# Kernel tuning notes

Hardware: AMD Instinct MI355X
Metric: run time of the kernel (lower is better)

## Reference

```python
import jax, jax.numpy as jnp
import numpy as np

GROUPS = 16
EPS = 1e-5


def _dcn_v2(x, offset, mask, weight):
    """Modulated deformable 3x3 conv, stride=1, pad=1, no bias.
    x: [B,C,H,W], offset: [B,18,H,W] (dy,dx interleaved per kernel point),
    mask: [B,9,H,W] (modulation scalars), weight: [O,C,3,3]."""
    B, C, H, W = x.shape
    O = weight.shape[0]
    K = 9
    # kernel-point displacements, row-major (kh, kw): k = kh*3 + kw
    ky = jnp.repeat(jnp.arange(3) - 1, 3).astype(x.dtype)   # [9]
    kx = jnp.tile(jnp.arange(3) - 1, 3).astype(x.dtype)      # [9]
    dy = offset[:, 0::2]  # [B,9,H,W]
    dx = offset[:, 1::2]  # [B,9,H,W]
    hh = jnp.arange(H, dtype=x.dtype)
    ww = jnp.arange(W, dtype=x.dtype)
    # sampling coordinates (stride=1, pad=1)
    ys = hh[None, None, :, None] + ky[None, :, None, None] + dy  # [B,9,H,W]
    xs = ww[None, None, None, :] + kx[None, :, None, None] + dx  # [B,9,H,W]

    y0 = jnp.floor(ys)
    x0 = jnp.floor(xs)
    wy1 = ys - y0
    wx1 = xs - x0
    y0i = y0.astype(jnp.int32)
    x0i = x0.astype(jnp.int32)

    flat = x.reshape(B, C, H * W)

    def gather(yi, xi, w):
        # yi, xi, w: [B,9,H,W]; zero-padding outside the image
        valid = (yi >= 0) & (yi < H) & (xi >= 0) & (xi < W)
        idx = jnp.clip(yi, 0, H - 1) * W + jnp.clip(xi, 0, W - 1)  # [B,9,H,W]
        g = jnp.take_along_axis(flat, idx.reshape(B, 1, K * H * W), axis=2)
        g = g.reshape(B, C, K, H, W)
        return g * (w * valid.astype(x.dtype))[:, None]  # [B,C,9,H,W]

    val = (gather(y0i,     x0i,     (1 - wy1) * (1 - wx1))
         + gather(y0i,     x0i + 1, (1 - wy1) * wx1)
         + gather(y0i + 1, x0i,     wy1 * (1 - wx1))
         + gather(y0i + 1, x0i + 1, wy1 * wx1))
    val = val * mask[:, None]  # modulation
    # implicit GEMM: [B,C,9,H,W] x [O,C,9] -> [B,O,H,W]
    return jnp.einsum('bckhw,ock->bohw', val, weight.reshape(O, C, K))


def _group_norm(x, gamma, beta):
    B, C, H, W = x.shape
    xg = x.reshape(B, GROUPS, C // GROUPS, H, W)
    mu = xg.mean(axis=(2, 3, 4), keepdims=True)
    var = xg.var(axis=(2, 3, 4), keepdims=True)
    xn = ((xg - mu) * jax.lax.rsqrt(var + EPS)).reshape(B, C, H, W)
    return xn * gamma[None, :, None, None] + beta[None, :, None, None]


def setup_inputs() -> dict:
    key = jax.random.key(0)
    k1, k2, k3, k4 = jax.random.split(key, 4)
    B, C, O, H, W = 8, 256, 256, 64, 64
    x = jax.random.normal(k1, (B, C, H, W), dtype=jnp.float32)
    offset = jax.random.normal(k2, (B, 18, H, W), dtype=jnp.float32)
    mask = jax.random.uniform(k3, (B, 9, H, W), dtype=jnp.float32)
    weight = jax.random.normal(k4, (O, C, 3, 3), dtype=jnp.float32) * (1.0 / np.sqrt(C * 9))
    gamma = jnp.ones((O,), dtype=jnp.float32)
    beta = jnp.zeros((O,), dtype=jnp.float32)
    return {"x": x, "offset": offset, "mask": mask, "weight": weight,
            "gamma": gamma, "beta": beta}


def reference(x, offset, mask, weight, gamma, beta):
    out = _dcn_v2(x, offset, mask, weight)
    return _group_norm(out, gamma, beta)
```

## Files before the change

kernel.cpp:

```cpp
#include <hip/hip_runtime.h>
#include <stdint.h>


#define B_ 8
#define C_ 256
#define O_ 256
#define H_ 64
#define W_ 64
#define HW_ 4096
#define KTOT 2304
#define GROUPS_ 16
#define EPS_ 1e-5f
#define NSTEP 36
#define VROW 72

typedef float  f32x4  __attribute__((ext_vector_type(4)));
typedef short  short8 __attribute__((ext_vector_type(8)));
typedef unsigned int   u32;
typedef unsigned short u16;

#define XT_BYTES (B_*HW_*C_*2)
#define WIMG_OFF  XT_BYTES
#define WIMG_BYTES (72*16*64*16)
#define STATS_OFF (WIMG_OFF + WIMG_BYTES)

__device__ __forceinline__ u32 bf16r(float f) {
    u32 u = __float_as_uint(f);
    return (u + 0x7fffu + ((u >> 16) & 1u)) >> 16;
}
__device__ __forceinline__ u32 pack_bf16x2(float lo, float hi) {
    return bf16r(lo) | (bf16r(hi) << 16);
}
__device__ __forceinline__ float bflo(u32 u) { return __uint_as_float(u << 16); }
__device__ __forceinline__ float bfhi(u32 u) { return __uint_as_float(u & 0xffff0000u); }

__global__ void k_prep(const float* __restrict__ x, u16* __restrict__ xt,
                       const float* __restrict__ w, u16* __restrict__ wimg) {
    __shared__ float tile[32][33];
    const int bid = blockIdx.x;
    const int tid = threadIdx.x;
    if (bid < 8192) {
        const int pt = bid & 127, ct = (bid >> 7) & 7, b = bid >> 10;
        const int tx = tid & 31, ty = tid >> 5;
        const int p = pt * 32 + tx;
#pragma unroll
        for (int i = 0; i < 4; ++i) {
            int c = ct * 32 + ty + i * 8;
            tile[ty + i * 8][tx] = x[(((size_t)b * C_ + c) << 12) + p];
        }
        __syncthreads();
        const int cp = tx & 15;
        const int ps = ty + (tx >> 4) * 8;
#pragma unroll
        for (int i = 0; i < 2; ++i) {
            const int pl = ps + i * 16;
            u32 v = pack_bf16x2(tile[2 * cp][pl], tile[2 * cp + 1][pl]);
            *(u32*)&xt[((((size_t)b << 12) + pt * 32 + pl) << 8) + ct * 32 + 2 * cp] = v;
        }
    } else {
        const int sub = bid - 8192;
        const int k  = sub >> 3;
        const int c0 = (sub & 7) * 32;
#pragma unroll
        for (int i = 0; i < 4; ++i) {
            const int item = tid + i * 256;
            const int lane = item & 63;
            const int frag = item >> 6;
            const int col = lane & 15, quad = lane >> 4;
            const int n = frag * 16 + col;
            const float* src = w + (size_t)n * KTOT + (size_t)(c0 + quad * 8) * 9 + k;
            u32 o[4];
#pragma unroll
            for (int j = 0; j < 4; ++j)
                o[j] = pack_bf16x2(src[(size_t)(2 * j) * 9], src[(size_t)(2 * j + 1) * 9]);
            *(uint4*)&wimg[((size_t)sub * 1024 + item) * 8] = *(uint4*)o;
        }
    }
}

__device__ __forceinline__ void issue_gather(const u16* __restrict__ xtb,
                                             const float* __restrict__ mwp,
                                             const int* __restrict__ mip,
                                             int c0, int gpos, int oct,
                                             uint4 g[8], f32x4& mw) {
    mw = *(const f32x4*)&mwp[gpos * 4];
    const int4 ix = *(const int4*)&mip[gpos * 4];
    const u16* cb = xtb + c0 + oct * 16;
    const u16* p0 = cb + ((size_t)ix.x << 8);
    const u16* p1 = cb + ((size_t)ix.y << 8);
    const u16* p2 = cb + ((size_t)ix.z << 8);
    const u16* p3 = cb + ((size_t)ix.w << 8);
    g[0] = *(const uint4*)p0; g[1] = *(const uint4*)(p0 + 8);
    g[2] = *(const uint4*)p1; g[3] = *(const uint4*)(p1 + 8);
    g[4] = *(const uint4*)p2; g[5] = *(const uint4*)(p2 + 8);
    g[6] = *(const uint4*)p3; g[7] = *(const uint4*)(p3 + 8);
}

__device__ __forceinline__ void interp_store(const uint4 g[8], f32x4 mw, u16* dst) {
    float s[16];
#pragma unroll
    for (int i = 0; i < 16; ++i) s[i] = 0.f;
    const float ww[4] = {mw.x, mw.y, mw.z, mw.w};
#pragma unroll
    for (int cr = 0; cr < 4; ++cr) {
        const float wg = ww[cr];
        const uint4 a = g[2 * cr], bq = g[2 * cr + 1];
        s[0] += wg * bflo(a.x);  s[1] += wg * bfhi(a.x);
        s[2] += wg * bflo(a.y);  s[3] += wg * bfhi(a.y);
        s[4] += wg * bflo(a.z);  s[5] += wg * bfhi(a.z);
        s[6] += wg * bflo(a.w);  s[7] += wg * bfhi(a.w);
        s[8]  += wg * bflo(bq.x); s[9]  += wg * bfhi(bq.x);
        s[10] += wg * bflo(bq.y); s[11] += wg * bfhi(bq.y);
        s[12] += wg * bflo(bq.z); s[13] += wg * bfhi(bq.z);
        s[14] += wg * bflo(bq.w); s[15] += wg * bfhi(bq.w);
    }
    uint4 pk0, pk1;
    pk0.x = pack_bf16x2(s[0], s[1]);   pk0.y = pack_bf16x2(s[2], s[3]);
    pk0.z = pack_bf16x2(s[4], s[5]);   pk0.w = pack_bf16x2(s[6], s[7]);
    pk1.x = pack_bf16x2(s[8], s[9]);   pk1.y = pack_bf16x2(s[10], s[11]);
    pk1.z = pack_bf16x2(s[12], s[13]); pk1.w = pack_bf16x2(s[14], s[15]);
    *(uint4*)dst = pk0;
    *(uint4*)(dst + 8) = pk1;
}

__device__ __forceinline__ void load_wfrags(const u16* __restrict__ wimg, int sub0,
                                            int wid, int lane, short8 bfp[8]) {
#pragma unroll
    for (int kc = 0; kc < 2; ++kc)
#pragma unroll
        for (int ni = 0; ni < 4; ++ni)
            bfp[kc * 4 + ni] = *(const short8*)
                &wimg[(((size_t)(sub0 + kc) * 16 + wid * 4 + ni) * 64 + lane) * 8];
}

__launch_bounds__(256, 2)
__global__ void k_dcn(const u16* __restrict__ xt, const u16* __restrict__ wimg,
                      const float* __restrict__ offp, const float* __restrict__ mskp,
                      float* __restrict__ out, float* __restrict__ stats) {
    __shared__ __align__(16) float meta_w[9 * 64 * 4];
    __shared__ __align__(16) int   meta_i[9 * 64 * 4];
    __shared__ __align__(16) u16   lds_v[2][64 * VROW];

    const int tid = threadIdx.x;
    const int gid = blockIdx.x;
    const int b   = gid & 7;
    const int m0  = (gid >> 3) * 64;
    const int lane = tid & 63, wid = tid >> 6;
    const int col = lane & 15, quad = lane >> 4;
    const int gpos = tid >> 2, oct = tid & 3;

    const u16* xtb = xt + ((size_t)b << 20);

    for (int it = tid; it < 576; it += 256) {
        const int pos = it & 63, k = it >> 6;
        const int pg = m0 + pos;
        const int hh = pg >> 6, wwi = pg & 63;
        const float dy = offp[((size_t)(b * 18 + 2 * k) << 12) + pg];
        const float dx = offp[((size_t)(b * 18 + 2 * k + 1) << 12) + pg];
        const float mv = mskp[((size_t)(b * 9 + k) << 12) + pg];
        const float ys = (float)(hh + (k / 3) - 1) + dy;
        const float xs = (float)(wwi + (k % 3) - 1) + dx;
        const float y0f = floorf(ys), x0f = floorf(xs);
        const int y0 = (int)y0f, x0 = (int)x0f;
        const float wy1 = ys - y0f, wx1 = xs - x0f;
        const float wy0 = 1.f - wy1, wx0 = 1.f - wx1;
        const int y1 = y0 + 1, x1 = x0 + 1;
        const float vy0 = (y0 >= 0 && y0 < H_) ? 1.f : 0.f;
        const float vy1 = (y1 >= 0 && y1 < H_) ? 1.f : 0.f;
        const float vx0 = (x0 >= 0 && x0 < W_) ? 1.f : 0.f;
        const float vx1 = (x1 >= 0 && x1 < W_) ? 1.f : 0.f;
        const int y0c = min(max(y0, 0), H_ - 1), y1c = min(max(y1, 0), H_ - 1);
        const int x0c = min(max(x0, 0), W_ - 1), x1c = min(max(x1, 0), W_ - 1);
        meta_w[it * 4 + 0] = mv * wy0 * wx0 * vy0 * vx0;
        meta_w[it * 4 + 1] = mv * wy0 * wx1 * vy0 * vx1;
        meta_w[it * 4 + 2] = mv * wy1 * wx0 * vy1 * vx0;
        meta_w[it * 4 + 3] = mv * wy1 * wx1 * vy1 * vx1;
        meta_i[it * 4 + 0] = y0c * W_ + x0c;
        meta_i[it * 4 + 1] = y0c * W_ + x1c;
        meta_i[it * 4 + 2] = y1c * W_ + x0c;
        meta_i[it * 4 + 3] = y1c * W_ + x1c;
    }
    __syncthreads();

    uint4 g[8]; f32x4 mw; short8 bfp[8];
    issue_gather(xtb, &meta_w[0], &meta_i[0], 0, gpos, oct, g, mw);
    load_wfrags(wimg, 0, wid, lane, bfp);
    interp_store(g, mw, &lds_v[0][gpos * VROW + oct * 16]);
    __syncthreads();

    f32x4 acc[4][4];
#pragma unroll
    for (int i = 0; i < 4; ++i)
#pragma unroll
        for (int j = 0; j < 4; ++j) acc[i][j] = (f32x4){0.f, 0.f, 0.f, 0.f};

#pragma unroll 2
    for (int s = 0; s < NSTEP; ++s) {
        const int p = s & 1;
        short8 bcur[8];
#pragma unroll
        for (int i = 0; i < 8; ++i) bcur[i] = bfp[i];

        const bool pf = (s + 1 < NSTEP);
        if (pf) {
            const int sn = s + 1;
            const int kn = sn >> 2, c0n = (sn & 3) * 64;
            issue_gather(xtb, &meta_w[kn * 256], &meta_i[kn * 256], c0n, gpos, oct, g, mw);
            load_wfrags(wimg, 2 * sn, wid, lane, bfp);
        }

#pragma unroll
        for (int kc = 0; kc < 2; ++kc) {
            short8 af[4];
#pragma unroll
            for (int mi = 0; mi < 4; ++mi)
                af[mi] = *(const short8*)
                    &lds_v[p][(mi * 16 + col) * VROW + kc * 32 + quad * 8];
#pragma unroll
            for (int mi = 0; mi < 4; ++mi)
#pragma unroll
                for (int ni = 0; ni < 4; ++ni)
                    acc[mi][ni] = __builtin_amdgcn_mfma_f32_16x16x32_bf16(
                        af[mi], bcur[kc * 4 + ni], acc[mi][ni], 0, 0, 0);
        }

        if (pf) interp_store(g, mw, &lds_v[1 - p][gpos * VROW + oct * 16]);
        __syncthreads();
    }

#pragma unroll
    for (int mi = 0; mi < 4; ++mi)
#pragma unroll
        for (int ni = 0; ni < 4; ++ni) {
            const int o  = wid * 64 + ni * 16 + col;
            const int pg = m0 + mi * 16 + quad * 4;
            *(f32x4*)(out + (((size_t)b * O_ + o) << 12) + pg) = acc[mi][ni];
        }

#pragma unroll
    for (int ni = 0; ni < 4; ++ni) {
        float s = 0.f, s2 = 0.f;
#pragma unroll
        for (int mi = 0; mi < 4; ++mi) {
            f32x4 v = acc[mi][ni];
            s  += v.x + v.y + v.z + v.w;
            s2 += v.x * v.x + v.y * v.y + v.z * v.z + v.w * v.w;
        }
#pragma unroll
        for (int d = 32; d > 0; d >>= 1) {
            s  += __shfl_xor(s, d, 64);
            s2 += __shfl_xor(s2, d, 64);
        }
        if (lane == 0) {
            const int gI = wid * 4 + ni;
            atomicAdd(&stats[b * GROUPS_ + gI], s);
            atomicAdd(&stats[128 + b * GROUPS_ + gI], s2);
        }
    }
}

__global__ void k_gn(float* __restrict__ out, const float* __restrict__ stats,
                     const float* __restrict__ gamma, const float* __restrict__ beta) {
    const int blk = blockIdx.x;
    const int b = blk >> 8, o = blk & 255;
    const int gI = b * GROUPS_ + (o >> 4);
    const float n = 65536.f;
    const float mean = stats[gI] / n;
    const float var  = stats[128 + gI] / n - mean * mean;
    const float inv  = rsqrtf(fmaxf(var, 0.f) + EPS_);
    const float scale = inv * gamma[o];
    const float shift = beta[o] - mean * scale;
    f32x4* p = (f32x4*)(out + ((size_t)blk << 12));
    const int t = threadIdx.x;
#pragma unroll
    for (int i = 0; i < 4; ++i) {
        f32x4 v = p[t + i * 256];
        p[t + i * 256] = v * scale + shift;
    }
}

extern "C" void kernel_launch(void* const* d_in, const int* in_sizes, int n_in,
                              void* d_out, int out_size, void* d_ws, size_t ws_size,
                              hipStream_t stream) {
    const float* x     = (const float*)d_in[0];
    const float* offp  = (const float*)d_in[1];
    const float* mskp  = (const float*)d_in[2];
    const float* w     = (const float*)d_in[3];
    const float* gamma = (const float*)d_in[4];
    const float* beta  = (const float*)d_in[5];
    float* outp = (float*)d_out;

    u16*   xt    = (u16*)d_ws;
    u16*   wimg  = (u16*)((char*)d_ws + WIMG_OFF);
    float* stats = (float*)((char*)d_ws + STATS_OFF);

    hipMemsetAsync(stats, 0, 1024, stream);
    k_prep<<<dim3(8192 + 72), dim3(256), 0, stream>>>(x, xt, w, wimg);
    k_dcn<<<dim3(512), dim3(256), 0, stream>>>(xt, wimg, offp, mskp, outp, stats);
    k_gn<<<dim3(2048), dim3(256), 0, stream>>>(outp, stats, gamma, beta);
}
```

Baseline: 201.3 us.

## Widen transpose tiles, pre-shift gather indices, truncate bf16 packing, custom barrier

The prep transpose now uses 64x64 tiles with float4 loads and 16-byte stores, cutting the block count fourfold and widening memory transactions. In the deformable conv kernel, gather indices are pre-shifted by the channel stride and the per-octet base pointer is hoisted, which removes address arithmetic from the inner loop. Interpolated values are packed to bf16 by truncation instead of round-to-nearest, which is cheaper but adds a small rounding bias. Weight fragments are now double-buffered explicitly, and __syncthreads is replaced by an inline-asm barrier that waits only on LDS counters, so global loads can stay in flight across the barrier.

Result: faster. 193.8 us (-3.8%).

```diff
diff --git a/kernel.cpp b/kernel.cpp
--- a/kernel.cpp
+++ b/kernel.cpp
@@ -31,34 +31,45 @@
 __device__ __forceinline__ u32 pack_bf16x2(float lo, float hi) {
     return bf16r(lo) | (bf16r(hi) << 16);
 }
+__device__ __forceinline__ u32 pack_trunc(float lo, float hi) {
+    return (__float_as_uint(hi) & 0xffff0000u) | (__float_as_uint(lo) >> 16);
+}
 __device__ __forceinline__ float bflo(u32 u) { return __uint_as_float(u << 16); }
 __device__ __forceinline__ float bfhi(u32 u) { return __uint_as_float(u & 0xffff0000u); }
 
+__device__ __forceinline__ void barrier_lds() {
+    asm volatile("s_waitcnt lgkmcnt(0)\n\ts_barrier" ::: "memory");
+}
+
 __global__ void k_prep(const float* __restrict__ x, u16* __restrict__ xt,
                        const float* __restrict__ w, u16* __restrict__ wimg) {
-    __shared__ float tile[32][33];
     const int bid = blockIdx.x;
     const int tid = threadIdx.x;
-    if (bid < 8192) {
-        const int pt = bid & 127, ct = (bid >> 7) & 7, b = bid >> 10;
-        const int tx = tid & 31, ty = tid >> 5;
-        const int p = pt * 32 + tx;
-#pragma unroll
-        for (int i = 0; i < 4; ++i) {
-            int c = ct * 32 + ty + i * 8;
-            tile[ty + i * 8][tx] = x[(((size_t)b * C_ + c) << 12) + p];
+    if (bid < 2048) {
+        __shared__ float tile[64][65];
+        const int b = bid >> 8, ct = (bid >> 6) & 3, pt = bid & 63;
+#pragma unroll
+        for (int pass = 0; pass < 4; ++pass) {
+            const int r  = (tid >> 4) + pass * 16;
+            const int pq = tid & 15;
+            const f32x4 v = *(const f32x4*)&x[(((size_t)(b * C_ + ct * 64 + r)) << 12)
+                                              + pt * 64 + pq * 4];
+            tile[r][pq * 4 + 0] = v.x;
+            tile[r][pq * 4 + 1] = v.y;
+            tile[r][pq * 4 + 2] = v.z;
+            tile[r][pq * 4 + 3] = v.w;
         }
         __syncthreads();
-        const int cp = tx & 15;
-        const int ps = ty + (tx >> 4) * 8;
-#pragma unroll
-        for (int i = 0; i < 2; ++i) {
-            const int pl = ps + i * 16;
-            u32 v = pack_bf16x2(tile[2 * cp][pl], tile[2 * cp + 1][pl]);
-            *(u32*)&xt[((((size_t)b << 12) + pt * 32 + pl) << 8) + ct * 32 + 2 * cp] = v;
-        }
+        const int pr = tid >> 2, cg = tid & 3;
+        u32 o[8];
+#pragma unroll
+        for (int j = 0; j < 8; ++j)
+            o[j] = pack_bf16x2(tile[cg * 16 + 2 * j][pr], tile[cg * 16 + 2 * j + 1][pr]);
+        u16* dst = &xt[(((size_t)b << 12) + pt * 64 + pr) * 256 + ct * 64 + cg * 16];
+        *(uint4*)dst       = *(uint4*)&o[0];
+        *(uint4*)(dst + 8) = *(uint4*)&o[4];
     } else {
-        const int sub = bid - 8192;
+        const int sub = bid - 2048;
         const int k  = sub >> 3;
         const int c0 = (sub & 7) * 32;
 #pragma unroll
@@ -78,18 +89,16 @@
     }
 }
 
-__device__ __forceinline__ void issue_gather(const u16* __restrict__ xtb,
+__device__ __forceinline__ void issue_gather(const u16* __restrict__ cb,
                                              const float* __restrict__ mwp,
                                              const int* __restrict__ mip,
-                                             int c0, int gpos, int oct,
-                                             uint4 g[8], f32x4& mw) {
+                                             int gpos, uint4 g[8], f32x4& mw) {
     mw = *(const f32x4*)&mwp[gpos * 4];
     const int4 ix = *(const int4*)&mip[gpos * 4];
-    const u16* cb = xtb + c0 + oct * 16;
-    const u16* p0 = cb + ((size_t)ix.x << 8);
-    const u16* p1 = cb + ((size_t)ix.y << 8);
-    const u16* p2 = cb + ((size_t)ix.z << 8);
-    const u16* p3 = cb + ((size_t)ix.w << 8);
+    const u16* p0 = cb + ix.x;
+    const u16* p1 = cb + ix.y;
+    const u16* p2 = cb + ix.z;
+    const u16* p3 = cb + ix.w;
     g[0] = *(const uint4*)p0; g[1] = *(const uint4*)(p0 + 8);
     g[2] = *(const uint4*)p1; g[3] = *(const uint4*)(p1 + 8);
     g[4] = *(const uint4*)p2; g[5] = *(const uint4*)(p2 + 8);
@@ -105,32 +114,32 @@
     for (int cr = 0; cr < 4; ++cr) {
         const float wg = ww[cr];
         const uint4 a = g[2 * cr], bq = g[2 * cr + 1];
-        s[0] += wg * bflo(a.x);  s[1] += wg * bfhi(a.x);
-        s[2] += wg * bflo(a.y);  s[3] += wg * bfhi(a.y);
-        s[4] += wg * bflo(a.z);  s[5] += wg * bfhi(a.z);
-        s[6] += wg * bflo(a.w);  s[7] += wg * bfhi(a.w);
+        s[0]  += wg * bflo(a.x);  s[1]  += wg * bfhi(a.x);
+        s[2]  += wg * bflo(a.y);  s[3]  += wg * bfhi(a.y);
+        s[4]  += wg * bflo(a.z);  s[5]  += wg * bfhi(a.z);
+        s[6]  += wg * bflo(a.w);  s[7]  += wg * bfhi(a.w);
         s[8]  += wg * bflo(bq.x); s[9]  += wg * bfhi(bq.x);
         s[10] += wg * bflo(bq.y); s[11] += wg * bfhi(bq.y);
         s[12] += wg * bflo(bq.z); s[13] += wg * bfhi(bq.z);
         s[14] += wg * bflo(bq.w); s[15] += wg * bfhi(bq.w);
     }
     uint4 pk0, pk1;
-    pk0.x = pack_bf16x2(s[0], s[1]);   pk0.y = pack_bf16x2(s[2], s[3]);
-    pk0.z = pack_bf16x2(s[4], s[5]);   pk0.w = pack_bf16x2(s[6], s[7]);
-    pk1.x = pack_bf16x2(s[8], s[9]);   pk1.y = pack_bf16x2(s[10], s[11]);
-    pk1.z = pack_bf16x2(s[12], s[13]); pk1.w = pack_bf16x2(s[14], s[15]);
+    pk0.x = pack_trunc(s[0], s[1]);   pk0.y = pack_trunc(s[2], s[3]);
+    pk0.z = pack_trunc(s[4], s[5]);   pk0.w = pack_trunc(s[6], s[7]);
+    pk1.x = pack_trunc(s[8], s[9]);   pk1.y = pack_trunc(s[10], s[11]);
+    pk1.z = pack_trunc(s[12], s[13]); pk1.w = pack_trunc(s[14], s[15]);
     *(uint4*)dst = pk0;
     *(uint4*)(dst + 8) = pk1;
 }
 
-__device__ __forceinline__ void load_wfrags(const u16* __restrict__ wimg, int sub0,
-                                            int wid, int lane, short8 bfp[8]) {
+__device__ __forceinline__ void load_wfrags(const u16* __restrict__ wimg, int s,
+                                            int wid, int lane, short8 bf[8]) {
 #pragma unroll
     for (int kc = 0; kc < 2; ++kc)
 #pragma unroll
         for (int ni = 0; ni < 4; ++ni)
-            bfp[kc * 4 + ni] = *(const short8*)
-                &wimg[(((size_t)(sub0 + kc) * 16 + wid * 4 + ni) * 64 + lane) * 8];
+            bf[kc * 4 + ni] = *(const short8*)
+                &wimg[(((size_t)(2 * s + kc) * 16 + wid * 4 + ni) * 64 + lane) * 8];
 }
 
 __launch_bounds__(256, 2)
@@ -175,16 +184,16 @@
         meta_w[it * 4 + 1] = mv * wy0 * wx1 * vy0 * vx1;
         meta_w[it * 4 + 2] = mv * wy1 * wx0 * vy1 * vx0;
         meta_w[it * 4 + 3] = mv * wy1 * wx1 * vy1 * vx1;
-        meta_i[it * 4 + 0] = y0c * W_ + x0c;
-        meta_i[it * 4 + 1] = y0c * W_ + x1c;
-        meta_i[it * 4 + 2] = y1c * W_ + x0c;
-        meta_i[it * 4 + 3] = y1c * W_ + x1c;
+        meta_i[it * 4 + 0] = (y0c * W_ + x0c) << 8;
+        meta_i[it * 4 + 1] = (y0c * W_ + x1c) << 8;
+        meta_i[it * 4 + 2] = (y1c * W_ + x0c) << 8;
+        meta_i[it * 4 + 3] = (y1c * W_ + x1c) << 8;
     }
     __syncthreads();
 
-    uint4 g[8]; f32x4 mw; short8 bfp[8];
-    issue_gather(xtb, &meta_w[0], &meta_i[0], 0, gpos, oct, g, mw);
-    load_wfrags(wimg, 0, wid, lane, bfp);
+    uint4 g[8]; f32x4 mw; short8 bf_cur[8], bf_nxt[8];
+    issue_gather(xtb + 0 + oct * 16, &meta_w[0], &meta_i[0], gpos, g, mw);
+    load_wfrags(wimg, 0, wid, lane, bf_cur);
     interp_store(g, mw, &lds_v[0][gpos * VROW + oct * 16]);
     __syncthreads();
 
@@ -197,16 +206,15 @@
 #pragma unroll 2
     for (int s = 0; s < NSTEP; ++s) {
         const int p = s & 1;
-        short8 bcur[8];
-#pragma unroll
-        for (int i = 0; i < 8; ++i) bcur[i] = bfp[i];
-
         const bool pf = (s + 1 < NSTEP);
+
+        if (pf) load_wfrags(wimg, s + 1, wid, lane, bf_nxt);
+
         if (pf) {
             const int sn = s + 1;
             const int kn = sn >> 2, c0n = (sn & 3) * 64;
-            issue_gather(xtb, &meta_w[kn * 256], &meta_i[kn * 256], c0n, gpos, oct, g, mw);
-            load_wfrags(wimg, 2 * sn, wid, lane, bfp);
+            issue_gather(xtb + c0n + oct * 16, &meta_w[kn * 256], &meta_i[kn * 256],
+                         gpos, g, mw);
         }
 
 #pragma unroll
@@ -221,11 +229,15 @@
 #pragma unroll
                 for (int ni = 0; ni < 4; ++ni)
                     acc[mi][ni] = __builtin_amdgcn_mfma_f32_16x16x32_bf16(
-                        af[mi], bcur[kc * 4 + ni], acc[mi][ni], 0, 0, 0);
+                        af[mi], bf_cur[kc * 4 + ni], acc[mi][ni], 0, 0, 0);
         }
 
         if (pf) interp_store(g, mw, &lds_v[1 - p][gpos * VROW + oct * 16]);
-        __syncthreads();
+
+        barrier_lds();
+
+#pragma unroll
+        for (int i = 0; i < 8; ++i) bf_cur[i] = bf_nxt[i];
     }
 
 #pragma unroll
@@ -295,7 +307,7 @@
     float* stats = (float*)((char*)d_ws + STATS_OFF);
 
     hipMemsetAsync(stats, 0, 1024, stream);
-    k_prep<<<dim3(8192 + 72), dim3(256), 0, stream>>>(x, xt, w, wimg);
+    k_prep<<<dim3(2048 + 72), dim3(256), 0, stream>>>(x, xt, w, wimg);
     k_dcn<<<dim3(512), dim3(256), 0, stream>>>(xt, wimg, offp, mskp, outp, stats);
     k_gn<<<dim3(2048), dim3(256), 0, stream>>>(outp, stats, gamma, beta);
 }
```
